# Kernel optimization log

Hardware: AMD Instinct MI355X
Metric: run time of the kernel (lower is better)

The kernel has to match this reference:

```python
import jax, jax.numpy as jnp
import numpy as np

N = 50000       # nodes
E = 800000      # edges (avg degree 16)
IN = 256        # in_features
HEAD = 4        # attention heads (conv1/conv2 out_channels)
F_OUT = 32      # mlp output features per head


def setup_inputs() -> dict:
    key = jax.random.key(0)
    ks = jax.random.split(key, 6)
    feat = jax.random.normal(ks[0], (N, IN), dtype=jnp.float32)
    edge_index = jax.random.randint(ks[1], (2, E), 0, N, dtype=jnp.int64)
    s = 1.0 / np.sqrt(IN)
    # mlp: Linear(IN -> HEAD*F_OUT)
    W_mlp = jax.random.uniform(ks[2], (IN, HEAD * F_OUT), jnp.float32, -s, s)
    b_mlp = jnp.zeros((HEAD * F_OUT,), jnp.float32)
    # conv1/conv2: 1x1 Conv1d(IN -> HEAD) == linear projection
    W1 = jax.random.uniform(ks[3], (HEAD, IN), jnp.float32, -s, s)
    b1 = jnp.zeros((HEAD,), jnp.float32)
    W2 = jax.random.uniform(ks[4], (HEAD, IN), jnp.float32, -s, s)
    b2 = jnp.zeros((HEAD,), jnp.float32)
    eps = jnp.zeros((1,), jnp.float32)  # trainable eps, init 0
    return {"feat": feat, "edge_index": edge_index, "W_mlp": W_mlp,
            "b_mlp": b_mlp, "W1": W1, "b1": b1, "W2": W2, "b2": b2,
            "eps": eps}


def reference(feat, edge_index, W_mlp, b_mlp, W1, b1, W2, b2, eps):
    n = feat.shape[0]
    head = W1.shape[0]
    # mlp: [N, IN] -> [N, head*F] -> [head, N, F]
    x = (feat @ W_mlp + b_mlp).reshape(n, head, -1).transpose(1, 0, 2)
    # 1x1 conv projections -> per-node attention logits [head, N]
    h1 = (feat @ W1.T + b1).T
    h2 = (feat @ W2.T + b2).T
    src = edge_index[0]  # edge[0]
    dst = edge_index[1]  # edge[1]
    # per-edge attention value, relu (dropout=0 -> identity): [head, E]
    v = jax.nn.relu(h1[:, src] + h2[:, dst])
    # gather neighbor features and weight: [head, E, F]
    msg = x[:, dst, :] * v[:, :, None]
    # scatter-add into destination nodes indexed by src: [N, head, F]
    agg = jax.ops.segment_sum(msg.transpose(1, 0, 2), src, num_segments=n)
    h_prime = agg.transpose(1, 0, 2) + eps[0] * x   # [head, N, F]
    # permute(1,0,2).reshape(N, -1) -> [N, head*F]
    return h_prime.transpose(1, 0, 2).reshape(n, -1)
```

## Files before the change

### kernel.cpp

```cpp
#include <hip/hip_runtime.h>

#define NN   50000
#define EE   800000
#define INF  256
#define COUT 128
#define BTROWS 144
#define PROJ_BLOCKS 782
#define CAP  52

typedef __attribute__((ext_vector_type(8))) short short8;
typedef __attribute__((ext_vector_type(4))) float f32x4;

__device__ __forceinline__ float b2f(unsigned short u) {
    union { unsigned int i; float f; } c;
    c.i = ((unsigned int)u) << 16;
    return c.f;
}
__device__ __forceinline__ unsigned short f2b(float f) {
    union { float f; unsigned int i; } c;
    c.f = f;
    unsigned int i = c.i;
    unsigned int lsb = (i >> 16) & 1u;
    i += 0x7fffu + lsb;
    return (unsigned short)(i >> 16);
}

__global__ __launch_bounds__(256) void zero_bt_kernel(
    const float* __restrict__ Wm, const float* __restrict__ W1,
    const float* __restrict__ W2,
    unsigned short* __restrict__ BT, int* __restrict__ cursor)
{
    const int t = threadIdx.x;
    if (blockIdx.x < 49) {
        const int idx = blockIdx.x * 256 + t;
        if (idx < 12500) ((int4*)cursor)[idx] = make_int4(0, 0, 0, 0);
    } else {
        const int n = blockIdx.x - 49;
        const int k = t;
        float v;
        if      (n < 128) v = Wm[k * COUT + n];
        else if (n < 132) v = W1[(n - 128) * INF + k];
        else if (n < 136) v = W2[(n - 132) * INF + k];
        else              v = 0.f;
        BT[n * INF + k] = f2b(v);
    }
}

#define LSTRIDE 72
__global__ __launch_bounds__(256) void proj_scatter_kernel(
    const float* __restrict__ feat,
    const unsigned short* __restrict__ BT,
    const float* __restrict__ bm,
    const float* __restrict__ b1,
    const float* __restrict__ b2,
    unsigned short* __restrict__ x_out,
    unsigned short* __restrict__ hh,
    const int* __restrict__ edge,
    int* __restrict__ cursor,
    unsigned short* __restrict__ sdst)
{
    __shared__ short lA[64 * LSTRIDE];
    __shared__ short lB[BTROWS * LSTRIDE];

    const int t = threadIdx.x;

    if (blockIdx.x >= PROJ_BLOCKS) {
        const int e = (blockIdx.x - PROJ_BLOCKS) * 256 + t;
        const int s = edge[e];
        const int d = edge[EE + e];
        const int p = atomicAdd(&cursor[s], 1);
        if (p < CAP) sdst[s * CAP + p] = (unsigned short)d;
        return;
    }

    const int lane  = t & 63;
    const int wave  = t >> 6;
    const int quad  = lane >> 4;
    const int col   = lane & 15;
    const int node0 = blockIdx.x * 64;

    f32x4 acc[9];
    #pragma unroll
    for (int i = 0; i < 9; i++) acc[i] = (f32x4){0.f, 0.f, 0.f, 0.f};

    for (int kc = 0; kc < 4; kc++) {
        const int k0 = kc * 64;
        #pragma unroll
        for (int p = 0; p < 4; p++) {
            const int idx = p * 256 + t;
            const int row = idx >> 4;
            const int c4  = idx & 15;
            const int grow = node0 + row;
            float4 f = make_float4(0.f, 0.f, 0.f, 0.f);
            if (grow < NN) f = *(const float4*)(feat + grow * INF + k0 + c4 * 4);
            short4 s;
            s.x = (short)f2b(f.x); s.y = (short)f2b(f.y);
            s.z = (short)f2b(f.z); s.w = (short)f2b(f.w);
            *(short4*)&lA[row * LSTRIDE + c4 * 4] = s;
        }
        #pragma unroll
        for (int p = 0; p < 5; p++) {
            const int idx = p * 256 + t;
            if (idx < (BTROWS * 64) / 8) {
                const int row = idx >> 3;
                const int c8  = idx & 7;
                uint4 u = *(const uint4*)(BT + row * INF + k0 + c8 * 8);
                *(uint4*)&lB[row * LSTRIDE + c8 * 8] = u;
            }
        }
        __syncthreads();

        #pragma unroll
        for (int ks = 0; ks < 2; ks++) {
            short8 a = *(const short8*)&lA[(wave * 16 + col) * LSTRIDE + ks * 32 + quad * 8];
            #pragma unroll
            for (int nt = 0; nt < 9; nt++) {
                short8 b = *(const short8*)&lB[(nt * 16 + col) * LSTRIDE + ks * 32 + quad * 8];
                acc[nt] = __builtin_amdgcn_mfma_f32_16x16x32_bf16(a, b, acc[nt], 0, 0, 0);
            }
        }
        __syncthreads();
    }

    const int rbase = node0 + wave * 16 + quad * 4;
    #pragma unroll
    for (int nt = 0; nt < 8; nt++) {
        const float bias = bm[nt * 16 + col];
        #pragma unroll
        for (int r = 0; r < 4; r++) {
            const int row = rbase + r;
            if (row < NN) x_out[row * COUT + nt * 16 + col] = f2b(acc[nt][r] + bias);
        }
    }
    if (col < 8) {
        const float bias = (col < 4) ? b1[col] : b2[col - 4];
        #pragma unroll
        for (int r = 0; r < 4; r++) {
            const int row = rbase + r;
            if (row < NN) hh[row * 8 + col] = f2b(acc[8][r] + bias);
        }
    }
}

__global__ __launch_bounds__(256) void accum_kernel(
    const int* __restrict__ cursor,
    const unsigned short* __restrict__ sdst,
    const unsigned short* __restrict__ x,
    const unsigned short* __restrict__ hh,
    const float* __restrict__ eps,
    float* __restrict__ out)
{
    const int lane = threadIdx.x & 63;
    const int node = blockIdx.x * 4 + (threadIdx.x >> 6);
    if (node >= NN) return;

    const int sub = lane & 7;
    const int g   = lane >> 3;
    const int h   = sub >> 1;

    const int deg = min(cursor[node], CAP);

    ushort4 h1u = *(const ushort4*)(hh + node * 8);

    int dv = 0;
    unsigned int vv01 = 0, vv23 = 0;
    if (lane < deg) {
        dv = (int)sdst[node * CAP + lane];
        ushort4 h2u = *(const ushort4*)(hh + dv * 8 + 4);
        const float v0 = b2f(h1u.x) + b2f(h2u.x);
        const float v1 = b2f(h1u.y) + b2f(h2u.y);
        const float v2 = b2f(h1u.z) + b2f(h2u.z);
        const float v3 = b2f(h1u.w) + b2f(h2u.w);
        vv01 = (unsigned int)f2b(v0) | ((unsigned int)f2b(v1) << 16);
        vv23 = (unsigned int)f2b(v2) | ((unsigned int)f2b(v3) << 16);
    }

    float acc[16];
    #pragma unroll
    for (int r = 0; r < 16; r++) acc[r] = 0.f;

    for (int i0 = 0; i0 < deg; i0 += 8) {
        const int idx = i0 + g;
        const int d = __shfl(dv, idx);
        const unsigned int u01 = (unsigned int)__shfl((int)vv01, idx);
        const unsigned int u23 = (unsigned int)__shfl((int)vv23, idx);
        unsigned short vb;
        if      (h == 0) vb = (unsigned short)(u01 & 0xffffu);
        else if (h == 1) vb = (unsigned short)(u01 >> 16);
        else if (h == 2) vb = (unsigned short)(u23 & 0xffffu);
        else             vb = (unsigned short)(u23 >> 16);
        const float v = b2f(vb);
        if (idx < deg && v > 0.f) {
            const unsigned short* xr = x + d * COUT + sub * 16;
            uint4 u0 = *(const uint4*)(xr);
            uint4 u1 = *(const uint4*)(xr + 8);
            acc[0]  = fmaf(b2f((unsigned short)(u0.x & 0xffffu)), v, acc[0]);
            acc[1]  = fmaf(b2f((unsigned short)(u0.x >> 16)),     v, acc[1]);
            acc[2]  = fmaf(b2f((unsigned short)(u0.y & 0xffffu)), v, acc[2]);
            acc[3]  = fmaf(b2f((unsigned short)(u0.y >> 16)),     v, acc[3]);
            acc[4]  = fmaf(b2f((unsigned short)(u0.z & 0xffffu)), v, acc[4]);
            acc[5]  = fmaf(b2f((unsigned short)(u0.z >> 16)),     v, acc[5]);
            acc[6]  = fmaf(b2f((unsigned short)(u0.w & 0xffffu)), v, acc[6]);
            acc[7]  = fmaf(b2f((unsigned short)(u0.w >> 16)),     v, acc[7]);
            acc[8]  = fmaf(b2f((unsigned short)(u1.x & 0xffffu)), v, acc[8]);
            acc[9]  = fmaf(b2f((unsigned short)(u1.x >> 16)),     v, acc[9]);
            acc[10] = fmaf(b2f((unsigned short)(u1.y & 0xffffu)), v, acc[10]);
            acc[11] = fmaf(b2f((unsigned short)(u1.y >> 16)),     v, acc[11]);
            acc[12] = fmaf(b2f((unsigned short)(u1.z & 0xffffu)), v, acc[12]);
            acc[13] = fmaf(b2f((unsigned short)(u1.z >> 16)),     v, acc[13]);
            acc[14] = fmaf(b2f((unsigned short)(u1.w & 0xffffu)), v, acc[14]);
            acc[15] = fmaf(b2f((unsigned short)(u1.w >> 16)),     v, acc[15]);
        }
    }

    #pragma unroll
    for (int r = 0; r < 16; r++) {
        acc[r] += __shfl_xor(acc[r], 8);
        acc[r] += __shfl_xor(acc[r], 16);
        acc[r] += __shfl_xor(acc[r], 32);
    }

    if (lane < 8) {
        const float e = eps[0];
        const unsigned short* xr = x + node * COUT + sub * 16;
        uint4 u0 = *(const uint4*)(xr);
        uint4 u1 = *(const uint4*)(xr + 8);
        unsigned int uu[8] = {u0.x, u0.y, u0.z, u0.w, u1.x, u1.y, u1.z, u1.w};
        #pragma unroll
        for (int q = 0; q < 8; q++) {
            acc[2 * q]     = fmaf(e, b2f((unsigned short)(uu[q] & 0xffffu)), acc[2 * q]);
            acc[2 * q + 1] = fmaf(e, b2f((unsigned short)(uu[q] >> 16)),     acc[2 * q + 1]);
        }
        float* o = out + node * COUT + sub * 16;
        #pragma unroll
        for (int q = 0; q < 4; q++)
            *(float4*)(o + q * 4) = make_float4(acc[4 * q], acc[4 * q + 1],
                                                acc[4 * q + 2], acc[4 * q + 3]);
    }
}

extern "C" void kernel_launch(void* const* d_in, const int* in_sizes, int n_in,
                              void* d_out, int out_size, void* d_ws, size_t ws_size,
                              hipStream_t stream) {
    const float* feat = (const float*)d_in[0];
    const int*   edge = (const int*)d_in[1];
    const float* Wm   = (const float*)d_in[2];
    const float* bm   = (const float*)d_in[3];
    const float* W1   = (const float*)d_in[4];
    const float* b1   = (const float*)d_in[5];
    const float* W2   = (const float*)d_in[6];
    const float* b2   = (const float*)d_in[7];
    const float* eps  = (const float*)d_in[8];

    char* ws = (char*)d_ws;
    unsigned short* x      = (unsigned short*)ws;
    unsigned short* hh     = (unsigned short*)(ws + 12800000);
    int*            cursor = (int*)(ws + 13600000);
    unsigned short* sdst   = (unsigned short*)(ws + 13800000);
    unsigned short* BT     = (unsigned short*)d_out;

    zero_bt_kernel<<<193, 256, 0, stream>>>(Wm, W1, W2, BT, cursor);
    proj_scatter_kernel<<<PROJ_BLOCKS + 3125, 256, 0, stream>>>(
        feat, BT, bm, b1, b2, x, hh, edge, cursor, sdst);
    accum_kernel<<<(NN + 3) / 4, 256, 0, stream>>>(cursor, sdst, x, hh, eps,
                                                   (float*)d_out);
}
```

Measured before the change: 186.1 us.

## Shard per-node adjacency cursors into 8 groups to cut atomic contention

The edge scatter now writes into 8 separate cursor/bucket arrays, one per group of edge blocks, each with a smaller per-node capacity. The aim is to spread atomic increments across more addresses so fewer threads contend on the same cursor. The accumulate kernel rebuilds each node's neighbour list with a wave prefix scan over the 8 group counts. In exchange it uses more workspace, has to zero 8x more cursors, and adds index arithmetic during accumulation. A fallback keeps the old path when the workspace is too small.

New measurement: 194.3 us. 1.04x slower.

```diff
diff --git a/kernel.cpp b/kernel.cpp
--- a/kernel.cpp
+++ b/kernel.cpp
@@ -7,6 +7,7 @@
 #define BTROWS 144
 #define PROJ_BLOCKS 782
 #define CAP  52
+#define CAP8 16
 
 typedef __attribute__((ext_vector_type(8))) short short8;
 typedef __attribute__((ext_vector_type(4))) float f32x4;
@@ -28,14 +29,15 @@
 __global__ __launch_bounds__(256) void zero_bt_kernel(
     const float* __restrict__ Wm, const float* __restrict__ W1,
     const float* __restrict__ W2,
-    unsigned short* __restrict__ BT, int* __restrict__ cursor)
+    unsigned short* __restrict__ BT, int* __restrict__ cursor, int nz)
 {
     const int t = threadIdx.x;
-    if (blockIdx.x < 49) {
+    const int zblocks = (nz + 255) / 256;
+    if ((int)blockIdx.x < zblocks) {
         const int idx = blockIdx.x * 256 + t;
-        if (idx < 12500) ((int4*)cursor)[idx] = make_int4(0, 0, 0, 0);
+        if (idx < nz) ((int4*)cursor)[idx] = make_int4(0, 0, 0, 0);
     } else {
-        const int n = blockIdx.x - 49;
+        const int n = blockIdx.x - zblocks;
         const int k = t;
         float v;
         if      (n < 128) v = Wm[k * COUT + n];
@@ -47,32 +49,14 @@
 }
 
 #define LSTRIDE 72
-__global__ __launch_bounds__(256) void proj_scatter_kernel(
-    const float* __restrict__ feat,
-    const unsigned short* __restrict__ BT,
-    const float* __restrict__ bm,
-    const float* __restrict__ b1,
+__device__ __forceinline__ void proj_body(
+    const float* __restrict__ feat, const unsigned short* __restrict__ BT,
+    const float* __restrict__ bm, const float* __restrict__ b1,
     const float* __restrict__ b2,
-    unsigned short* __restrict__ x_out,
-    unsigned short* __restrict__ hh,
-    const int* __restrict__ edge,
-    int* __restrict__ cursor,
-    unsigned short* __restrict__ sdst)
-{
-    __shared__ short lA[64 * LSTRIDE];
-    __shared__ short lB[BTROWS * LSTRIDE];
-
-    const int t = threadIdx.x;
-
-    if (blockIdx.x >= PROJ_BLOCKS) {
-        const int e = (blockIdx.x - PROJ_BLOCKS) * 256 + t;
-        const int s = edge[e];
-        const int d = edge[EE + e];
-        const int p = atomicAdd(&cursor[s], 1);
-        if (p < CAP) sdst[s * CAP + p] = (unsigned short)d;
-        return;
-    }
-
+    unsigned short* __restrict__ x_out, unsigned short* __restrict__ hh,
+    short* lA, short* lB)
+{
+    const int t     = threadIdx.x;
     const int lane  = t & 63;
     const int wave  = t >> 6;
     const int quad  = lane >> 4;
@@ -142,6 +126,177 @@
     }
 }
 
+__global__ __launch_bounds__(256) void proj_scatter_g_kernel(
+    const float* __restrict__ feat, const unsigned short* __restrict__ BT,
+    const float* __restrict__ bm, const float* __restrict__ b1,
+    const float* __restrict__ b2,
+    unsigned short* __restrict__ x_out, unsigned short* __restrict__ hh,
+    const int* __restrict__ edge,
+    int* __restrict__ cursor8,
+    unsigned short* __restrict__ sdst8)
+{
+    __shared__ short lA[64 * LSTRIDE];
+    __shared__ short lB[BTROWS * LSTRIDE];
+    const int t = threadIdx.x;
+
+    if (blockIdx.x >= PROJ_BLOCKS) {
+        const int b2_ = blockIdx.x - PROJ_BLOCKS;
+        const int e   = b2_ * 256 + t;
+        const int g   = b2_ & 7;
+        const int s   = edge[e];
+        const int d   = edge[EE + e];
+        const int gs  = g * NN + s;
+        const int p   = atomicAdd(&cursor8[gs], 1);
+        if (p < CAP8) sdst8[gs * CAP8 + p] = (unsigned short)d;
+        return;
+    }
+    proj_body(feat, BT, bm, b1, b2, x_out, hh, lA, lB);
+}
+
+__global__ __launch_bounds__(256) void accum_g_kernel(
+    const int* __restrict__ cursor8,
+    const unsigned short* __restrict__ sdst8,
+    const unsigned short* __restrict__ x,
+    const unsigned short* __restrict__ hh,
+    const float* __restrict__ eps,
+    float* __restrict__ out)
+{
+    const int lane = threadIdx.x & 63;
+    const int node = blockIdx.x * 4 + (threadIdx.x >> 6);
+    if (node >= NN) return;
+
+    const int sub = lane & 7;
+    const int g   = lane >> 3;
+    const int h   = sub >> 1;
+
+    int C = 0, S = 0;
+    if (lane < 8) {
+        const int gs = lane * NN + node;
+        C = min(cursor8[gs], CAP8);
+        S = gs * CAP8;
+    }
+    int incl = C;
+    #pragma unroll
+    for (int off = 1; off < 8; off <<= 1) {
+        int u = __shfl_up(incl, off);
+        if (lane >= off) incl += u;
+    }
+    const int P = incl - C;
+    const int deg = __shfl(incl, 7);
+
+    const ushort4 h1u = *(const ushort4*)(hh + node * 8);
+
+    float acc[16];
+    #pragma unroll
+    for (int r = 0; r < 16; r++) acc[r] = 0.f;
+
+    for (int c0 = 0; c0 < deg; c0 += 64) {
+        const int j = c0 + lane;
+        int addr = 0;
+        #pragma unroll
+        for (int gg = 0; gg < 8; gg++) {
+            const int Pg = __shfl(P, gg);
+            const int Sg = __shfl(S, gg);
+            if (Pg <= j) addr = Sg + (j - Pg);
+        }
+        int dv = 0;
+        unsigned int vv01 = 0, vv23 = 0;
+        if (j < deg) {
+            dv = (int)sdst8[addr];
+            ushort4 h2u = *(const ushort4*)(hh + dv * 8 + 4);
+            const float v0 = b2f(h1u.x) + b2f(h2u.x);
+            const float v1 = b2f(h1u.y) + b2f(h2u.y);
+            const float v2 = b2f(h1u.z) + b2f(h2u.z);
+            const float v3 = b2f(h1u.w) + b2f(h2u.w);
+            vv01 = (unsigned int)f2b(v0) | ((unsigned int)f2b(v1) << 16);
+            vv23 = (unsigned int)f2b(v2) | ((unsigned int)f2b(v3) << 16);
+        }
+        const int m = min(64, deg - c0);
+        for (int i0 = 0; i0 < m; i0 += 8) {
+            const int idx = i0 + g;
+            const int d = __shfl(dv, idx);
+            const unsigned int u01 = (unsigned int)__shfl((int)vv01, idx);
+            const unsigned int u23 = (unsigned int)__shfl((int)vv23, idx);
+            unsigned short vb;
+            if      (h == 0) vb = (unsigned short)(u01 & 0xffffu);
+            else if (h == 1) vb = (unsigned short)(u01 >> 16);
+            else if (h == 2) vb = (unsigned short)(u23 & 0xffffu);
+            else             vb = (unsigned short)(u23 >> 16);
+            const float v = b2f(vb);
+            if (idx < m && v > 0.f) {
+                const unsigned short* xr = x + d * COUT + sub * 16;
+                uint4 u0 = *(const uint4*)(xr);
+                uint4 u1 = *(const uint4*)(xr + 8);
+                acc[0]  = fmaf(b2f((unsigned short)(u0.x & 0xffffu)), v, acc[0]);
+                acc[1]  = fmaf(b2f((unsigned short)(u0.x >> 16)),     v, acc[1]);
+                acc[2]  = fmaf(b2f((unsigned short)(u0.y & 0xffffu)), v, acc[2]);
+                acc[3]  = fmaf(b2f((unsigned short)(u0.y >> 16)),     v, acc[3]);
+                acc[4]  = fmaf(b2f((unsigned short)(u0.z & 0xffffu)), v, acc[4]);
+                acc[5]  = fmaf(b2f((unsigned short)(u0.z >> 16)),     v, acc[5]);
+                acc[6]  = fmaf(b2f((unsigned short)(u0.w & 0xffffu)), v, acc[6]);
+                acc[7]  = fmaf(b2f((unsigned short)(u0.w >> 16)),     v, acc[7]);
+                acc[8]  = fmaf(b2f((unsigned short)(u1.x & 0xffffu)), v, acc[8]);
+                acc[9]  = fmaf(b2f((unsigned short)(u1.x >> 16)),     v, acc[9]);
+                acc[10] = fmaf(b2f((unsigned short)(u1.y & 0xffffu)), v, acc[10]);
+                acc[11] = fmaf(b2f((unsigned short)(u1.y >> 16)),     v, acc[11]);
+                acc[12] = fmaf(b2f((unsigned short)(u1.z & 0xffffu)), v, acc[12]);
+                acc[13] = fmaf(b2f((unsigned short)(u1.z >> 16)),     v, acc[13]);
+                acc[14] = fmaf(b2f((unsigned short)(u1.w & 0xffffu)), v, acc[14]);
+                acc[15] = fmaf(b2f((unsigned short)(u1.w >> 16)),     v, acc[15]);
+            }
+        }
+    }
+
+    #pragma unroll
+    for (int r = 0; r < 16; r++) {
+        acc[r] += __shfl_xor(acc[r], 8);
+        acc[r] += __shfl_xor(acc[r], 16);
+        acc[r] += __shfl_xor(acc[r], 32);
+    }
+
+    if (lane < 8) {
+        const float e = eps[0];
+        const unsigned short* xr = x + node * COUT + sub * 16;
+        uint4 u0 = *(const uint4*)(xr);
+        uint4 u1 = *(const uint4*)(xr + 8);
+        unsigned int uu[8] = {u0.x, u0.y, u0.z, u0.w, u1.x, u1.y, u1.z, u1.w};
+        #pragma unroll
+        for (int q = 0; q < 8; q++) {
+            acc[2 * q]     = fmaf(e, b2f((unsigned short)(uu[q] & 0xffffu)), acc[2 * q]);
+            acc[2 * q + 1] = fmaf(e, b2f((unsigned short)(uu[q] >> 16)),     acc[2 * q + 1]);
+        }
+        float* o = out + node * COUT + sub * 16;
+        #pragma unroll
+        for (int q = 0; q < 4; q++)
+            *(float4*)(o + q * 4) = make_float4(acc[4 * q], acc[4 * q + 1],
+                                                acc[4 * q + 2], acc[4 * q + 3]);
+    }
+}
+
+__global__ __launch_bounds__(256) void proj_scatter_kernel(
+    const float* __restrict__ feat, const unsigned short* __restrict__ BT,
+    const float* __restrict__ bm, const float* __restrict__ b1,
+    const float* __restrict__ b2,
+    unsigned short* __restrict__ x_out, unsigned short* __restrict__ hh,
+    const int* __restrict__ edge,
+    int* __restrict__ cursor,
+    unsigned short* __restrict__ sdst)
+{
+    __shared__ short lA[64 * LSTRIDE];
+    __shared__ short lB[BTROWS * LSTRIDE];
+    const int t = threadIdx.x;
+
+    if (blockIdx.x >= PROJ_BLOCKS) {
+        const int e = (blockIdx.x - PROJ_BLOCKS) * 256 + t;
+        const int s = edge[e];
+        const int d = edge[EE + e];
+        const int p = atomicAdd(&cursor[s], 1);
+        if (p < CAP) sdst[s * CAP + p] = (unsigned short)d;
+        return;
+    }
+    proj_body(feat, BT, bm, b1, b2, x_out, hh, lA, lB);
+}
+
 __global__ __launch_bounds__(256) void accum_kernel(
     const int* __restrict__ cursor,
     const unsigned short* __restrict__ sdst,
@@ -159,8 +314,7 @@
     const int h   = sub >> 1;
 
     const int deg = min(cursor[node], CAP);
-
-    ushort4 h1u = *(const ushort4*)(hh + node * 8);
+    const ushort4 h1u = *(const ushort4*)(hh + node * 8);
 
     int dv = 0;
     unsigned int vv01 = 0, vv23 = 0;
@@ -253,15 +407,27 @@
     const float* eps  = (const float*)d_in[8];
 
     char* ws = (char*)d_ws;
-    unsigned short* x      = (unsigned short*)ws;
-    unsigned short* hh     = (unsigned short*)(ws + 12800000);
-    int*            cursor = (int*)(ws + 13600000);
-    unsigned short* sdst   = (unsigned short*)(ws + 13800000);
-    unsigned short* BT     = (unsigned short*)d_out;
-
-    zero_bt_kernel<<<193, 256, 0, stream>>>(Wm, W1, W2, BT, cursor);
-    proj_scatter_kernel<<<PROJ_BLOCKS + 3125, 256, 0, stream>>>(
-        feat, BT, bm, b1, b2, x, hh, edge, cursor, sdst);
-    accum_kernel<<<(NN + 3) / 4, 256, 0, stream>>>(cursor, sdst, x, hh, eps,
-                                                   (float*)d_out);
-}
+    unsigned short* x  = (unsigned short*)ws;
+    unsigned short* hh = (unsigned short*)(ws + 12800000);
+    unsigned short* BT = (unsigned short*)d_out;
+
+    if (ws_size >= 28100000) {
+        int*            cursor8 = (int*)(ws + 13600000);
+        unsigned short* sdst8   = (unsigned short*)(ws + 15200000);
+        const int nz = (8 * NN) / 4;
+        zero_bt_kernel<<<(nz + 255) / 256 + BTROWS, 256, 0, stream>>>(Wm, W1, W2, BT, cursor8, nz);
+        proj_scatter_g_kernel<<<PROJ_BLOCKS + 3125, 256, 0, stream>>>(
+            feat, BT, bm, b1, b2, x, hh, edge, cursor8, sdst8);
+        accum_g_kernel<<<(NN + 3) / 4, 256, 0, stream>>>(cursor8, sdst8, x, hh, eps,
+                                                         (float*)d_out);
+    } else {
+        int*            cursor = (int*)(ws + 13600000);
+        unsigned short* sdst   = (unsigned short*)(ws + 13800000);
+        const int nz = 12500;
+        zero_bt_kernel<<<49 + BTROWS, 256, 0, stream>>>(Wm, W1, W2, BT, cursor, nz);
+        proj_scatter_kernel<<<PROJ_BLOCKS + 3125, 256, 0, stream>>>(
+            feat, BT, bm, b1, b2, x, hh, edge, cursor, sdst);
+        accum_kernel<<<(NN + 3) / 4, 256, 0, stream>>>(cursor, sdst, x, hh, eps,
+                                                       (float*)d_out);
+    }
+}
```
